# Performance work log

Measured on AMD Instinct MI355X. Metric: run time of the kernel, lower is better.

The kernel has to match this reference:

```python
import jax, jax.numpy as jnp
import numpy as np
import math

B, L, D, H = 2, 2048, 1024, 16
DH = D // H  # 64


def setup_inputs() -> dict:
    key = jax.random.key(0)
    ks = jax.random.split(key, 8)
    s = 1.0 / math.sqrt(D)
    return {
        "query": jax.random.normal(ks[0], (B, L, D), dtype=jnp.float32),
        "key": jax.random.normal(ks[1], (B, L, D), dtype=jnp.float32),
        "value": jax.random.normal(ks[2], (B, L, D), dtype=jnp.float32),
        "attn_mask": jax.random.bernoulli(ks[3], 0.1, (B, L, L)),  # True = masked
        "Wq": jax.random.normal(ks[4], (D, D), dtype=jnp.float32) * s,
        "Wk": jax.random.normal(ks[5], (D, D), dtype=jnp.float32) * s,
        "Wv": jax.random.normal(ks[6], (D, D), dtype=jnp.float32) * s,
        "Wo": jax.random.normal(ks[7], (D, D), dtype=jnp.float32) * s,
    }


def reference(query, key, value, attn_mask, Wq, Wk, Wv, Wo):
    # torch nn.Linear computes x @ W.T (bias=False here)
    def shape(x):
        b, l, _ = x.shape
        return x.reshape(b, l, H, DH).transpose(0, 2, 1, 3)  # [B,H,L,DH]

    q = shape(query @ Wq.T) / jnp.sqrt(jnp.float32(DH))
    k = shape(key @ Wk.T)
    v = shape(value @ Wv.T)

    scores = jnp.einsum("bhqd,bhkd->bhqk", q, k)  # [B,H,Q,K]
    if attn_mask is not None:
        scores = jnp.where(attn_mask[:, None, :, :], jnp.float32(-1e18), scores)
    attn = jax.nn.softmax(scores, axis=-1)
    # dropout p=0.0 (eval/deterministic) -> identity
    context = jnp.einsum("bhqk,bhkd->bhqd", attn, v)
    context = context.transpose(0, 2, 1, 3).reshape(query.shape[0], -1, D)
    output = context @ Wo.T
    top_attn = attn[:, 0, :, :]
    return output, top_attn
```

## Files before the change

kernel.cpp:

```cpp
#include <hip/hip_runtime.h>

#define BB 2
#define LL 2048
#define DD 1024
#define HH 16
#define DHH 64

typedef _Float16 f16;
typedef _Float16 f16x8 __attribute__((ext_vector_type(8)));
typedef _Float16 f16x4 __attribute__((ext_vector_type(4)));
typedef _Float16 f16x2 __attribute__((ext_vector_type(2)));
typedef float f32x4 __attribute__((ext_vector_type(4)));
typedef unsigned long long u64;

#define VWAIT(N) asm volatile("s_waitcnt vmcnt(" #N ")" ::: "memory")
#define SB0() __builtin_amdgcn_sched_barrier(0)

__device__ __forceinline__ void gload_lds16(const void* g, void* l) {
    __builtin_amdgcn_global_load_lds(
        (const __attribute__((address_space(1))) void*)g,
        (__attribute__((address_space(3))) void*)l, 16, 0, 0);
}

__device__ __forceinline__ f16x4 cvt4f(float4 v) {
    f16x4 o;
    o[0] = (f16)v.x; o[1] = (f16)v.y; o[2] = (f16)v.z; o[3] = (f16)v.w;
    return o;
}

__global__ void prep(const float* __restrict__ q, const float* __restrict__ k,
                     const float* __restrict__ v, const int* __restrict__ msk,
                     const float* __restrict__ wq, const float* __restrict__ wk,
                     const float* __restrict__ wv, const float* __restrict__ wo,
                     f16* __restrict__ bufQ, f16* __restrict__ bufK, f16* __restrict__ bufV,
                     f16* __restrict__ wh, u64* __restrict__ Mp, float scq) {
    const int tid = threadIdx.x;
    const int y = blockIdx.y;
    if (y == 0) {
        const int lane = tid & 63;
        int w = (blockIdx.x * 256 + tid) >> 6;
        const int nw = (1024 * 256) >> 6;
        for (; w < BB * LL * 32; w += nw) {
            int mv = msk[(size_t)w * 64 + lane];
            u64 bits = __ballot(mv != 0);
            if (lane == 0) {
                const int kt = w & 31;
                const int bq = w >> 5;
                const int qq = bq & 2047, b = bq >> 11;
                Mp[((size_t)b * 32 + kt) * LL + qq] = bits;
            }
        }
    } else if (y == 1) {
        int i = blockIdx.x * 256 + tid;
        const int stride = 1024 * 256;
        for (; i < 4 * 262144; i += stride) {
            const int sel = i >> 18, j = i & 262143;
            const float* s = sel == 0 ? wq : sel == 1 ? wk : sel == 2 ? wv : wo;
            ((f16x4*)wh)[i] = cvt4f(((const float4*)s)[j]);
        }
    } else {
        const float* s = y == 2 ? q : y == 3 ? k : v;
        f16* o = y == 2 ? bufQ : y == 3 ? bufK : bufV;
        const float sc = y == 2 ? scq : 1.0f;
        int i = blockIdx.x * 256 + tid;
        const int stride = 1024 * 256;
        for (; i < (int)(BB * LL * DD / 4); i += stride) {
            float4 vv = ((const float4*)s)[i];
            vv.x *= sc; vv.y *= sc; vv.z *= sc; vv.w *= sc;
            ((f16x4*)o)[i] = cvt4f(vv);
        }
    }
}

__global__ void cvt_kernel(const float* __restrict__ src, f16* __restrict__ dst, int n4, float sc) {
    int i = blockIdx.x * blockDim.x + threadIdx.x;
    const int stride = gridDim.x * blockDim.x;
    for (; i < n4; i += stride) {
        float4 v = ((const float4*)src)[i];
        v.x *= sc; v.y *= sc; v.z *= sc; v.w *= sc;
        ((f16x4*)dst)[i] = cvt4f(v);
    }
}
__global__ void cvt4_kernel(const float* __restrict__ a, const float* __restrict__ b,
                            const float* __restrict__ c, const float* __restrict__ d,
                            f16* __restrict__ dst, int n4) {
    const float* s = blockIdx.y == 0 ? a : blockIdx.y == 1 ? b : blockIdx.y == 2 ? c : d;
    f16* o = dst + (size_t)blockIdx.y * n4 * 4;
    int i = blockIdx.x * blockDim.x + threadIdx.x;
    const int stride = gridDim.x * blockDim.x;
    for (; i < n4; i += stride)
        ((f16x4*)o)[i] = cvt4f(((const float4*)s)[i]);
}
__global__ void pack_mask(const int* __restrict__ mask, u64* __restrict__ out, int nwords) {
    const int lane = threadIdx.x & 63;
    int w = (blockIdx.x * blockDim.x + threadIdx.x) >> 6;
    const int nw = (gridDim.x * blockDim.x) >> 6;
    for (; w < nwords; w += nw) {
        int mv = mask[(size_t)w * 64 + lane];
        u64 bits = __ballot(mv != 0);
        if (lane == 0) {
            const int kt = w & 31;
            const int bq = w >> 5;
            const int qq = bq & 2047, b = bq >> 11;
            out[((size_t)b * 32 + kt) * LL + qq] = bits;
        }
    }
}

__device__ __forceinline__ void gemm_core(const f16* __restrict__ A, const f16* __restrict__ W,
                                          f16* __restrict__ C, int z, int xb, int yb, char* lds) {
    const int tid = threadIdx.x, wid = tid >> 6, lane = tid & 63;
    const int m0 = yb * 128, n0 = xb * 128;
    const int lq = lane & 15, lg = lane >> 4;
    const int wm = (wid >> 1) << 6, wn = (wid & 1) << 6;
    f32x4 acc[4][4] = {};

    #pragma unroll
    for (int t = 0; t < 2; ++t)
        #pragma unroll
        for (int j = 0; j < 2; ++j) {
            const int ldsoff = (wid * 2 + j) << 10;
            const int o = ldsoff + lane * 16;
            const int row = o >> 6, c8 = (o >> 4) & 3;
            gload_lds16(A + (size_t)(m0 + row) * DD + t * 32 + c8 * 8, lds + t * 8192 + ldsoff);
            gload_lds16(W + (size_t)(n0 + row) * DD + t * 32 + c8 * 8, lds + 24576 + t * 8192 + ldsoff);
        }

    for (int kt = 0; kt < 32; ++kt) {
        VWAIT(4);
        SB0();
        __builtin_amdgcn_s_barrier();
        SB0();
        {
            const int nk = (kt + 2 < 32) ? kt + 2 : 31;
            const int nb = (kt + 2) % 3;
            #pragma unroll
            for (int j = 0; j < 2; ++j) {
                const int ldsoff = (wid * 2 + j) << 10;
                const int o = ldsoff + lane * 16;
                const int row = o >> 6, c8 = (o >> 4) & 3;
                gload_lds16(A + (size_t)(m0 + row) * DD + nk * 32 + c8 * 8,
                            lds + nb * 8192 + ldsoff);
                gload_lds16(W + (size_t)(n0 + row) * DD + nk * 32 + c8 * 8,
                            lds + 24576 + nb * 8192 + ldsoff);
            }
        }
        SB0();

        const int cb = kt % 3;
        const char* Ab = lds + cb * 8192;
        const char* Bb = lds + 24576 + cb * 8192;
        f16x8 af[4], bf[4];
        #pragma unroll
        for (int m = 0; m < 4; ++m)
            af[m] = *(const f16x8*)(Ab + (wm + m * 16 + lq) * 64 + lg * 16);
        #pragma unroll
        for (int n = 0; n < 4; ++n)
            bf[n] = *(const f16x8*)(Bb + (wn + n * 16 + lq) * 64 + lg * 16);
        __builtin_amdgcn_s_setprio(1);
        #pragma unroll
        for (int m = 0; m < 4; ++m)
            #pragma unroll
            for (int n = 0; n < 4; ++n)
                acc[m][n] = __builtin_amdgcn_mfma_f32_16x16x32_f16(af[m], bf[n], acc[m][n], 0, 0, 0);
        __builtin_amdgcn_s_setprio(0);
    }

    #pragma unroll
    for (int m = 0; m < 4; ++m)
        #pragma unroll
        for (int n = 0; n < 4; ++n)
            #pragma unroll
            for (int r = 0; r < 4; ++r) {
                const int row = m0 + wm + m * 16 + lg * 4 + r;
                const int col = n0 + wn + n * 16 + lq;
                const float val = acc[m][n][r];
                if (z < 2) {
                    C[(size_t)row * DD + col] = (f16)val;
                } else {
                    const int b = row >> 11, l = row & 2047;
                    const int h = col >> 6, dh = col & 63;
                    C[((size_t)((b * HH + h) * DHH + dh) << 11) + l] = (f16)val;
                }
            }
}

__global__ __launch_bounds__(256) void gemm_qkv(
        const f16* __restrict__ A0, const f16* __restrict__ A1, const f16* __restrict__ A2,
        const f16* __restrict__ W0, const f16* __restrict__ W1, const f16* __restrict__ W2,
        f16* __restrict__ C0, f16* __restrict__ C1, f16* __restrict__ C2) {
    __shared__ __align__(16) char lds[49152];
    const int bid = blockIdx.x;
    const int xcd = bid & 7, j = bid >> 3;
    const int p = xcd * 12 + (j >> 3);
    const int xb = j & 7;
    const int z = p >> 5, yb = p & 31;
    const f16* A = z == 0 ? A0 : z == 1 ? A1 : A2;
    const f16* W = z == 0 ? W0 : z == 1 ? W1 : W2;
    f16* C       = z == 0 ? C0 : z == 1 ? C1 : C2;
    gemm_core(A, W, C, z, xb, yb, lds);
}

__global__ __launch_bounds__(256) void gemm_one(const f16* __restrict__ A, const f16* __restrict__ W,
                                                f16* __restrict__ C, int z) {
    __shared__ __align__(16) char lds[49152];
    gemm_core(A, W, C, z, blockIdx.x, blockIdx.y, lds);
}

template<bool TOPF16>
__global__ __launch_bounds__(256) void finale(const f16* __restrict__ A, const f16* __restrict__ W,
                                              float* __restrict__ C, float* __restrict__ top,
                                              const void* __restrict__ src,
                                              const float* __restrict__ linvp) {
    __shared__ __align__(16) char lds[36864];
    const int tid = threadIdx.x;
    if (blockIdx.x >= 512) {
        int i = (blockIdx.x - 512) * 256 + tid;
        const int stride = 1024 * 256;
        if (TOPF16) {
            const f16x8* s8 = (const f16x8*)src;
            const int n = (int)((size_t)BB * LL * LL / 8);
            for (; i < n; i += stride) {
                f16x8 v = s8[i];
                const float linv = linvp[(i * 8) >> 11];
                float4 a, bq;
                a.x = (float)v[0] * linv; a.y = (float)v[1] * linv;
                a.z = (float)v[2] * linv; a.w = (float)v[3] * linv;
                bq.x = (float)v[4] * linv; bq.y = (float)v[5] * linv;
                bq.z = (float)v[6] * linv; bq.w = (float)v[7] * linv;
                ((float4*)top)[i * 2] = a;
                ((float4*)top)[i * 2 + 1] = bq;
            }
        } else {
            const int n = (int)((size_t)BB * LL * LL / 4);
            for (; i < n; i += stride) {
                float4 v = ((const float4*)top)[i];
                const float linv = linvp[(i * 4) >> 11];
                v.x = __builtin_amdgcn_exp2f(v.x) * linv;
                v.y = __builtin_amdgcn_exp2f(v.y) * linv;
                v.z = __builtin_amdgcn_exp2f(v.z) * linv;
                v.w = __builtin_amdgcn_exp2f(v.w) * linv;
                ((float4*)top)[i] = v;
            }
        }
        return;
    }
    const int bid = blockIdx.x;
    const int xcd = bid & 7, j = bid >> 3;
    const int yb = xcd * 4 + (j >> 4);
    const int xb = j & 15;
    const int wid = tid >> 6, lane = tid & 63;
    const int m0 = yb * 128, n0 = xb * 64;
    const int lq = lane & 15, lg = lane >> 4;
    const int wm = wid * 32;
    f32x4 acc[2][4] = {};

    #pragma unroll
    for (int t = 0; t < 2; ++t) {
        #pragma unroll
        for (int j2 = 0; j2 < 2; ++j2) {
            const int o = (j2 * 256 + tid) * 16;
            const int row = o >> 6, c8 = (o >> 4) & 3;
            gload_lds16(A + (size_t)(m0 + row) * DD + t * 32 + c8 * 8,
                        lds + t * 8192 + j2 * 4096 + (wid << 10));
        }
        {
            const int o = tid * 16;
            const int row = o >> 6, c8 = (o >> 4) & 3;
            gload_lds16(W + (size_t)(n0 + row) * DD + t * 32 + c8 * 8,
                        lds + 24576 + t * 4096 + (wid << 10));
        }
    }

    for (int kt = 0; kt < 32; ++kt) {
        VWAIT(3);
        SB0();
        __builtin_amdgcn_s_barrier();
        SB0();
        {
            const int nk = (kt + 2 < 32) ? kt + 2 : 31;
            const int nb = (kt + 2) % 3;
            #pragma unroll
            for (int j2 = 0; j2 < 2; ++j2) {
                const int o = (j2 * 256 + tid) * 16;
                const int row = o >> 6, c8 = (o >> 4) & 3;
                gload_lds16(A + (size_t)(m0 + row) * DD + nk * 32 + c8 * 8,
                            lds + nb * 8192 + j2 * 4096 + (wid << 10));
            }
            {
                const int o = tid * 16;
                const int row = o >> 6, c8 = (o >> 4) & 3;
                gload_lds16(W + (size_t)(n0 + row) * DD + nk * 32 + c8 * 8,
                            lds + 24576 + nb * 4096 + (wid << 10));
            }
        }
        SB0();

        const int cb = kt % 3;
        const char* Ab = lds + cb * 8192;
        const char* Bb = lds + 24576 + cb * 4096;
        f16x8 af[2], bf[4];
        #pragma unroll
        for (int m = 0; m < 2; ++m)
            af[m] = *(const f16x8*)(Ab + (wm + m * 16 + lq) * 64 + lg * 16);
        #pragma unroll
        for (int n = 0; n < 4; ++n)
            bf[n] = *(const f16x8*)(Bb + (n * 16 + lq) * 64 + lg * 16);
        __builtin_amdgcn_s_setprio(1);
        #pragma unroll
        for (int m = 0; m < 2; ++m)
            #pragma unroll
            for (int n = 0; n < 4; ++n)
                acc[m][n] = __builtin_amdgcn_mfma_f32_16x16x32_f16(af[m], bf[n], acc[m][n], 0, 0, 0);
        __builtin_amdgcn_s_setprio(0);
    }

    #pragma unroll
    for (int m = 0; m < 2; ++m)
        #pragma unroll
        for (int n = 0; n < 4; ++n)
            #pragma unroll
            for (int r = 0; r < 4; ++r) {
                const int row = m0 + wm + m * 16 + lg * 4 + r;
                const int col = n0 + n * 16 + lq;
                C[(size_t)row * DD + col] = acc[m][n][r];
            }
}

template<bool TOPF16>
__global__ __launch_bounds__(256) void attn_fwd(const f16* __restrict__ Qp, const f16* __restrict__ Kp,
                                                const f16* __restrict__ VTp,
                                                const u64* __restrict__ Mp,
                                                f16* __restrict__ Op, void* __restrict__ topout,
                                                float* __restrict__ statsLinv) {
    extern __shared__ char lds[];
    const int tid = threadIdx.x, wid = tid >> 6, lane = tid & 63;
    const int lq = lane & 15, lg = lane >> 4;
    const int bid = blockIdx.x;
    const int xcd = bid & 7, j = bid >> 3;
    const int bh = xcd * 4 + (j >> 5);
    const int qt = j & 31;
    const int b = bh >> 4, h = bh & 15;
    const bool topblk = (h == 0);
    const int qrow = qt * 64 + wid * 16 + lq;

    f16x8 qf[2];
    #pragma unroll
    for (int kk = 0; kk < 2; ++kk)
        qf[kk] = *(const f16x8*)(Qp + (size_t)(b * LL + qrow) * DD + h * 64 + (kk * 4 + lg) * 8);

    {
        #pragma unroll
        for (int jj = 0; jj < 2; ++jj) {
            const int o = (wid * 2 + jj) * 1024 + lane * 16;
            const int row = o >> 7, sc = ((o >> 4) & 7) ^ (row & 7);
            gload_lds16(Kp + (size_t)(b * LL + row) * DD + h * 64 + sc * 8,
                        lds + 8192 + (wid * 2 + jj) * 1024);
            gload_lds16(VTp + (size_t)((b * HH + h) * DHH + row) * LL + sc * 8,
                        lds + 24576 + (wid * 2 + jj) * 1024);
        }
    }

    float lsum = 0.f;
    f32x4 acc[4] = {};

    for (int kt = 0; kt < 32; ++kt) {
        if (topblk && kt > 0) { VWAIT(4); } else { VWAIT(0); }
        SB0();
        __builtin_amdgcn_s_barrier();
        SB0();
        const u64 cm = Mp[((size_t)b * 32 + kt) * LL + qrow];
        SB0();
        {
            const int nk = (kt + 1 < 32) ? kt + 1 : 31;
            const int nb = (kt + 1) & 1;
            #pragma unroll
            for (int jj = 0; jj < 2; ++jj) {
                const int o = (wid * 2 + jj) * 1024 + lane * 16;
                const int row = o >> 7, sc = ((o >> 4) & 7) ^ (row & 7);
                gload_lds16(Kp + (size_t)(b * LL + nk * 64 + row) * DD + h * 64 + sc * 8,
                            lds + 8192 + nb * 8192 + (wid * 2 + jj) * 1024);
                gload_lds16(VTp + (size_t)((b * HH + h) * DHH + row) * LL + nk * 64 + sc * 8,
                            lds + 24576 + nb * 8192 + (wid * 2 + jj) * 1024);
            }
        }
        SB0();

        const int cb = kt & 1;
        const char* Kb = lds + 8192 + cb * 8192;
        const char* Vb = lds + 24576 + cb * 8192;

        f32x4 s[4] = {};
        __builtin_amdgcn_s_setprio(1);
        #pragma unroll
        for (int f = 0; f < 4; ++f)
            #pragma unroll
            for (int kk = 0; kk < 2; ++kk) {
                const int co = (((kk * 4 + lg) ^ (lq & 7)) << 4);
                f16x8 kf = *(const f16x8*)(Kb + (f * 16 + lq) * 128 + co);
                s[f] = __builtin_amdgcn_mfma_f32_16x16x32_f16(kf, qf[kk], s[f], 0, 0, 0);
            }
        __builtin_amdgcn_s_setprio(0);

        const u64 wsh = cm >> (lg * 4);
        const unsigned lo = (unsigned)wsh, hi = (unsigned)(wsh >> 32);
        f16x4 ph[4];
        #pragma unroll
        for (int f = 0; f < 4; ++f) {
            const unsigned nib = ((f < 2) ? (lo >> (f * 16)) : (hi >> ((f - 2) * 16))) & 0xFu;
            #pragma unroll
            for (int r = 0; r < 4; ++r)
                if (nib & (1u << r)) s[f][r] = -1e18f;
            const float p0 = __builtin_amdgcn_exp2f(s[f][0]);
            const float p1 = __builtin_amdgcn_exp2f(s[f][1]);
            const float p2 = __builtin_amdgcn_exp2f(s[f][2]);
            const float p3 = __builtin_amdgcn_exp2f(s[f][3]);
            lsum += (p0 + p1) + (p2 + p3);
            f16x2 pa = __builtin_bit_cast(f16x2, __builtin_amdgcn_cvt_pkrtz(p0, p1));
            f16x2 pb = __builtin_bit_cast(f16x2, __builtin_amdgcn_cvt_pkrtz(p2, p3));
            ph[f][0] = pa[0]; ph[f][1] = pa[1]; ph[f][2] = pb[0]; ph[f][3] = pb[1];
        }

        if (topblk) {
            if (TOPF16) {
                f16* T = (f16*)topout;
                #pragma unroll
                for (int f = 0; f < 4; ++f)
                    *(f16x4*)(T + ((size_t)b * LL + qrow) * LL + kt * 64 + f * 16 + lg * 4) = ph[f];
            } else {
                float* T = (float*)topout;
                #pragma unroll
                for (int f = 0; f < 4; ++f)
                    *(f32x4*)(T + ((size_t)b * LL + qrow) * LL + kt * 64 + f * 16 + lg * 4) = s[f];
            }
        }

        #pragma unroll
        for (int f = 0; f < 4; ++f) {
            const int chunk = f * 2 + (lg >> 1);
            const int bo = ((chunk ^ (lq & 7)) << 4) + (lg & 1) * 8;
            *(f16x4*)(lds + (wid << 11) + lq * 128 + bo) = ph[f];
        }

        __builtin_amdgcn_s_setprio(1);
        #pragma unroll
        for (int kk = 0; kk < 2; ++kk) {
            const int co = (((kk * 4 + lg) ^ (lq & 7)) << 4);
            f16x8 pf = *(const f16x8*)(lds + (wid << 11) + lq * 128 + co);
            #pragma unroll
            for (int f = 0; f < 4; ++f) {
                f16x8 vf = *(const f16x8*)(Vb + (f * 16 + lq) * 128 + co);
                acc[f] = __builtin_amdgcn_mfma_f32_16x16x32_f16(vf, pf, acc[f], 0, 0, 0);
            }
        }
        __builtin_amdgcn_s_setprio(0);
    }

    lsum += __shfl_xor(lsum, 16);
    lsum += __shfl_xor(lsum, 32);
    const float linv = 1.f / lsum;
    #pragma unroll
    for (int f = 0; f < 4; ++f) {
        f16x4 ov;
        #pragma unroll
        for (int r = 0; r < 4; ++r) ov[r] = (f16)(acc[f][r] * linv);
        *(f16x4*)(Op + (size_t)(b * LL + qrow) * DD + h * 64 + f * 16 + lg * 4) = ov;
    }
    if (topblk && lg == 0) statsLinv[(size_t)b * LL + qrow] = linv;
}

extern "C" void kernel_launch(void* const* d_in, const int* in_sizes, int n_in,
                              void* d_out, int out_size, void* d_ws, size_t ws_size,
                              hipStream_t stream) {
    const float* q   = (const float*)d_in[0];
    const float* k   = (const float*)d_in[1];
    const float* v   = (const float*)d_in[2];
    const int*   msk = (const int*)d_in[3];
    const float* wq  = (const float*)d_in[4];
    const float* wk  = (const float*)d_in[5];
    const float* wv  = (const float*)d_in[6];
    const float* wo  = (const float*)d_in[7];
    float* out = (float*)d_out;

    const size_t NX = (size_t)BB * LL * DD;
    const size_t NW = (size_t)DD * DD;
    const int NMW = BB * LL * (LL / 64);
    const size_t NXo = NX;
    const float SCQ = 0.125f * 1.4426950408889634f;
    const int ALDS = 40960;

    f16* ws = (f16*)d_ws;
    const size_t needed = (6 * NX + 4 * NW) * 2 + (size_t)NMW * 8 + (size_t)BB * LL * 4;
    const bool fused = ws_size >= needed;

    if (fused) {
        f16* bufQ = ws;
        f16* bufK = bufQ + NX;
        f16* bufV = bufK + NX;
        f16* Op   = bufQ;
        f16* topP = bufK;
        f16* wh   = bufV + NX;
        f16* wqh = wh, *wkh = wh + NW, *wvh = wh + 2 * NW, *woh = wh + 3 * NW;
        f16* Qp  = wh + 4 * NW;
        f16* Kp  = Qp + NX;
        f16* VTp = Kp + NX;
        u64* Mp  = (u64*)(VTp + NX);
        float* statsLinv = (float*)(Mp + NMW);

        prep<<<dim3(1024, 5), 256, 0, stream>>>(q, k, v, msk, wq, wk, wv, wo,
                                                bufQ, bufK, bufV, wh, Mp, SCQ);
        gemm_qkv<<<768, 256, 0, stream>>>(bufQ, bufK, bufV, wqh, wkh, wvh, Qp, Kp, VTp);
        attn_fwd<true><<<1024, 256, ALDS, stream>>>(Qp, Kp, VTp, Mp, Op, topP, statsLinv);
        finale<true><<<1536, 256, 0, stream>>>(Op, woh, out, out + NXo, topP, statsLinv);
    } else {
        f16* bufA = ws;
        f16* wh   = bufA + NX;
        f16* wqh = wh, *wkh = wh + NW, *wvh = wh + 2 * NW, *woh = wh + 3 * NW;
        f16* Qp  = wh + 4 * NW;
        f16* Kp  = Qp + NX;
        f16* VTp = Kp + NX;
        u64* Mp  = (u64*)(VTp + NX);
        float* statsLinv = (float*)(Mp + NMW);

        pack_mask<<<256, 256, 0, stream>>>(msk, Mp, NMW);
        cvt4_kernel<<<dim3(128, 4), 256, 0, stream>>>(wq, wk, wv, wo, wh, (int)(NW / 4));
        cvt_kernel<<<2048, 256, 0, stream>>>(q, bufA, (int)(NX / 4), SCQ);
        gemm_one<<<dim3(8, 32), 256, 0, stream>>>(bufA, wqh, Qp, 0);
        cvt_kernel<<<2048, 256, 0, stream>>>(k, bufA, (int)(NX / 4), 1.f);
        gemm_one<<<dim3(8, 32), 256, 0, stream>>>(bufA, wkh, Kp, 1);
        cvt_kernel<<<2048, 256, 0, stream>>>(v, bufA, (int)(NX / 4), 1.f);
        gemm_one<<<dim3(8, 32), 256, 0, stream>>>(bufA, wvh, VTp, 2);
        attn_fwd<false><<<1024, 256, ALDS, stream>>>(Qp, Kp, VTp, Mp, bufA,
                                                     out + NXo, statsLinv);
        finale<false><<<1536, 256, 0, stream>>>(bufA, woh, out, out + NXo, out + NXo, statsLinv);
    }
}
```

Baseline: 161.2 us.

## Use 128-row query tiles with 8 waves and a 4-deep K/V pipeline

The attention kernel now runs 512 threads per block covering 128 query rows, so each K/V tile loaded into LDS serves twice as many queries. The loop handles two 64-key tiles per barrier with a 4-slot ring buffer, prefetching two tiles ahead. LDS per block doubles to 80 KB, set via hipFuncSetAttribute. This halves the block count to 512 and may lower occupancy.

```diff
diff --git a/kernel.cpp b/kernel.cpp
--- a/kernel.cpp
+++ b/kernel.cpp
@@ -328,7 +328,7 @@
 }
 
 template<bool TOPF16>
-__global__ __launch_bounds__(256) void attn_fwd(const f16* __restrict__ Qp, const f16* __restrict__ Kp,
+__global__ __launch_bounds__(512) void attn_fwd(const f16* __restrict__ Qp, const f16* __restrict__ Kp,
                                                 const f16* __restrict__ VTp,
                                                 const u64* __restrict__ Mp,
                                                 f16* __restrict__ Op, void* __restrict__ topout,
@@ -338,122 +338,123 @@
     const int lq = lane & 15, lg = lane >> 4;
     const int bid = blockIdx.x;
     const int xcd = bid & 7, j = bid >> 3;
-    const int bh = xcd * 4 + (j >> 5);
-    const int qt = j & 31;
+    const int bh = xcd * 4 + (j >> 4);
+    const int qt = j & 15;
     const int b = bh >> 4, h = bh & 15;
     const bool topblk = (h == 0);
-    const int qrow = qt * 64 + wid * 16 + lq;
+    const int qrow = qt * 128 + wid * 16 + lq;
+
+    const int srow = tid >> 3;
+    const int ssc = ((tid & 7) ^ (srow & 7));
+    const f16* ksrc = Kp + (size_t)(b * LL + srow) * DD + h * 64 + ssc * 8;
+    const f16* vsrc = VTp + (size_t)((b * HH + h) * DHH + srow) * LL + ssc * 8;
+    char* kdst = lds + 16384 + (wid << 10);
+    char* vdst = lds + 49152 + (wid << 10);
 
     f16x8 qf[2];
     #pragma unroll
     for (int kk = 0; kk < 2; ++kk)
         qf[kk] = *(const f16x8*)(Qp + (size_t)(b * LL + qrow) * DD + h * 64 + (kk * 4 + lg) * 8);
 
-    {
-        #pragma unroll
-        for (int jj = 0; jj < 2; ++jj) {
-            const int o = (wid * 2 + jj) * 1024 + lane * 16;
-            const int row = o >> 7, sc = ((o >> 4) & 7) ^ (row & 7);
-            gload_lds16(Kp + (size_t)(b * LL + row) * DD + h * 64 + sc * 8,
-                        lds + 8192 + (wid * 2 + jj) * 1024);
-            gload_lds16(VTp + (size_t)((b * HH + h) * DHH + row) * LL + sc * 8,
-                        lds + 24576 + (wid * 2 + jj) * 1024);
-        }
+    #pragma unroll
+    for (int t = 0; t < 2; ++t) {
+        gload_lds16(ksrc + (size_t)t * 64 * DD, kdst + t * 8192);
+        gload_lds16(vsrc + t * 64, vdst + t * 8192);
     }
 
     float lsum = 0.f;
     f32x4 acc[4] = {};
 
-    for (int kt = 0; kt < 32; ++kt) {
-        if (topblk && kt > 0) { VWAIT(4); } else { VWAIT(0); }
+    for (int it = 0; it < 16; ++it) {
+        const int kt0 = it * 2;
+        if (topblk && it > 0) { VWAIT(8); } else { VWAIT(0); }
         SB0();
         __builtin_amdgcn_s_barrier();
         SB0();
-        const u64 cm = Mp[((size_t)b * 32 + kt) * LL + qrow];
-        SB0();
-        {
-            const int nk = (kt + 1 < 32) ? kt + 1 : 31;
-            const int nb = (kt + 1) & 1;
-            #pragma unroll
-            for (int jj = 0; jj < 2; ++jj) {
-                const int o = (wid * 2 + jj) * 1024 + lane * 16;
-                const int row = o >> 7, sc = ((o >> 4) & 7) ^ (row & 7);
-                gload_lds16(Kp + (size_t)(b * LL + nk * 64 + row) * DD + h * 64 + sc * 8,
-                            lds + 8192 + nb * 8192 + (wid * 2 + jj) * 1024);
-                gload_lds16(VTp + (size_t)((b * HH + h) * DHH + row) * LL + nk * 64 + sc * 8,
-                            lds + 24576 + nb * 8192 + (wid * 2 + jj) * 1024);
-            }
-        }
-        SB0();
-
-        const int cb = kt & 1;
-        const char* Kb = lds + 8192 + cb * 8192;
-        const char* Vb = lds + 24576 + cb * 8192;
-
-        f32x4 s[4] = {};
-        __builtin_amdgcn_s_setprio(1);
-        #pragma unroll
-        for (int f = 0; f < 4; ++f)
+        const u64 cm0 = Mp[((size_t)b * 32 + kt0) * LL + qrow];
+        const u64 cm1 = Mp[((size_t)b * 32 + kt0 + 1) * LL + qrow];
+        SB0();
+        #pragma unroll
+        for (int t = 0; t < 2; ++t) {
+            const int nk = (kt0 + 2 + t < 32) ? kt0 + 2 + t : 31;
+            const int nb = (kt0 + 2 + t) & 3;
+            gload_lds16(ksrc + (size_t)nk * 64 * DD, kdst + nb * 8192);
+            gload_lds16(vsrc + nk * 64, vdst + nb * 8192);
+        }
+        SB0();
+
+        #pragma unroll
+        for (int t = 0; t < 2; ++t) {
+            const int cb = (kt0 + t) & 3;
+            const char* Kb = lds + 16384 + cb * 8192;
+            const char* Vb = lds + 49152 + cb * 8192;
+            const u64 cm = t == 0 ? cm0 : cm1;
+
+            f32x4 s[4] = {};
+            __builtin_amdgcn_s_setprio(1);
+            #pragma unroll
+            for (int f = 0; f < 4; ++f)
+                #pragma unroll
+                for (int kk = 0; kk < 2; ++kk) {
+                    const int co = (((kk * 4 + lg) ^ (lq & 7)) << 4);
+                    f16x8 kf = *(const f16x8*)(Kb + (f * 16 + lq) * 128 + co);
+                    s[f] = __builtin_amdgcn_mfma_f32_16x16x32_f16(kf, qf[kk], s[f], 0, 0, 0);
+                }
+            __builtin_amdgcn_s_setprio(0);
+
+            const u64 wsh = cm >> (lg * 4);
+            const unsigned lo = (unsigned)wsh, hi = (unsigned)(wsh >> 32);
+            f16x4 ph[4];
+            #pragma unroll
+            for (int f = 0; f < 4; ++f) {
+                const unsigned nib = ((f < 2) ? (lo >> (f * 16)) : (hi >> ((f - 2) * 16))) & 0xFu;
+                #pragma unroll
+                for (int r = 0; r < 4; ++r)
+                    if (nib & (1u << r)) s[f][r] = -1e18f;
+                const float p0 = __builtin_amdgcn_exp2f(s[f][0]);
+                const float p1 = __builtin_amdgcn_exp2f(s[f][1]);
+                const float p2 = __builtin_amdgcn_exp2f(s[f][2]);
+                const float p3 = __builtin_amdgcn_exp2f(s[f][3]);
+                lsum += (p0 + p1) + (p2 + p3);
+                f16x2 pa = __builtin_bit_cast(f16x2, __builtin_amdgcn_cvt_pkrtz(p0, p1));
+                f16x2 pb = __builtin_bit_cast(f16x2, __builtin_amdgcn_cvt_pkrtz(p2, p3));
+                ph[f][0] = pa[0]; ph[f][1] = pa[1]; ph[f][2] = pb[0]; ph[f][3] = pb[1];
+            }
+
+            if (topblk) {
+                if (TOPF16) {
+                    f16* T = (f16*)topout;
+                    #pragma unroll
+                    for (int f = 0; f < 4; ++f)
+                        *(f16x4*)(T + ((size_t)b * LL + qrow) * LL + (kt0 + t) * 64 + f * 16 + lg * 4) = ph[f];
+                } else {
+                    float* T = (float*)topout;
+                    #pragma unroll
+                    for (int f = 0; f < 4; ++f)
+                        *(f32x4*)(T + ((size_t)b * LL + qrow) * LL + (kt0 + t) * 64 + f * 16 + lg * 4) = s[f];
+                }
+            }
+
+            #pragma unroll
+            for (int f = 0; f < 4; ++f) {
+                const int chunk = f * 2 + (lg >> 1);
+                const int bo = ((chunk ^ (lq & 7)) << 4) + (lg & 1) * 8;
+                *(f16x4*)(lds + (wid << 11) + lq * 128 + bo) = ph[f];
+            }
+
+            __builtin_amdgcn_s_setprio(1);
             #pragma unroll
             for (int kk = 0; kk < 2; ++kk) {
                 const int co = (((kk * 4 + lg) ^ (lq & 7)) << 4);
-                f16x8 kf = *(const f16x8*)(Kb + (f * 16 + lq) * 128 + co);
-                s[f] = __builtin_amdgcn_mfma_f32_16x16x32_f16(kf, qf[kk], s[f], 0, 0, 0);
-            }
-        __builtin_amdgcn_s_setprio(0);
-
-        const u64 wsh = cm >> (lg * 4);
-        const unsigned lo = (unsigned)wsh, hi = (unsigned)(wsh >> 32);
-        f16x4 ph[4];
-        #pragma unroll
-        for (int f = 0; f < 4; ++f) {
-            const unsigned nib = ((f < 2) ? (lo >> (f * 16)) : (hi >> ((f - 2) * 16))) & 0xFu;
-            #pragma unroll
-            for (int r = 0; r < 4; ++r)
-                if (nib & (1u << r)) s[f][r] = -1e18f;
-            const float p0 = __builtin_amdgcn_exp2f(s[f][0]);
-            const float p1 = __builtin_amdgcn_exp2f(s[f][1]);
-            const float p2 = __builtin_amdgcn_exp2f(s[f][2]);
-            const float p3 = __builtin_amdgcn_exp2f(s[f][3]);
-            lsum += (p0 + p1) + (p2 + p3);
-            f16x2 pa = __builtin_bit_cast(f16x2, __builtin_amdgcn_cvt_pkrtz(p0, p1));
-            f16x2 pb = __builtin_bit_cast(f16x2, __builtin_amdgcn_cvt_pkrtz(p2, p3));
-            ph[f][0] = pa[0]; ph[f][1] = pa[1]; ph[f][2] = pb[0]; ph[f][3] = pb[1];
-        }
-
-        if (topblk) {
-            if (TOPF16) {
-                f16* T = (f16*)topout;
+                f16x8 pf = *(const f16x8*)(lds + (wid << 11) + lq * 128 + co);
                 #pragma unroll
-                for (int f = 0; f < 4; ++f)
-                    *(f16x4*)(T + ((size_t)b * LL + qrow) * LL + kt * 64 + f * 16 + lg * 4) = ph[f];
-            } else {
-                float* T = (float*)topout;
-                #pragma unroll
-                for (int f = 0; f < 4; ++f)
-                    *(f32x4*)(T + ((size_t)b * LL + qrow) * LL + kt * 64 + f * 16 + lg * 4) = s[f];
-            }
-        }
-
-        #pragma unroll
-        for (int f = 0; f < 4; ++f) {
-            const int chunk = f * 2 + (lg >> 1);
-            const int bo = ((chunk ^ (lq & 7)) << 4) + (lg & 1) * 8;
-            *(f16x4*)(lds + (wid << 11) + lq * 128 + bo) = ph[f];
-        }
-
-        __builtin_amdgcn_s_setprio(1);
-        #pragma unroll
-        for (int kk = 0; kk < 2; ++kk) {
-            const int co = (((kk * 4 + lg) ^ (lq & 7)) << 4);
-            f16x8 pf = *(const f16x8*)(lds + (wid << 11) + lq * 128 + co);
-            #pragma unroll
-            for (int f = 0; f < 4; ++f) {
-                f16x8 vf = *(const f16x8*)(Vb + (f * 16 + lq) * 128 + co);
-                acc[f] = __builtin_amdgcn_mfma_f32_16x16x32_f16(vf, pf, acc[f], 0, 0, 0);
-            }
-        }
-        __builtin_amdgcn_s_setprio(0);
+                for (int f = 0; f < 4; ++f) {
+                    f16x8 vf = *(const f16x8*)(Vb + (f * 16 + lq) * 128 + co);
+                    acc[f] = __builtin_amdgcn_mfma_f32_16x16x32_f16(vf, pf, acc[f], 0, 0, 0);
+                }
+            }
+            __builtin_amdgcn_s_setprio(0);
+        }
     }
 
     lsum += __shfl_xor(lsum, 16);
@@ -487,7 +488,12 @@
     const int NMW = BB * LL * (LL / 64);
     const size_t NXo = NX;
     const float SCQ = 0.125f * 1.4426950408889634f;
-    const int ALDS = 40960;
+    const int ALDS = 81920;
+
+    hipFuncSetAttribute(reinterpret_cast<const void*>(attn_fwd<true>),
+                        hipFuncAttributeMaxDynamicSharedMemorySize, ALDS);
+    hipFuncSetAttribute(reinterpret_cast<const void*>(attn_fwd<false>),
+                        hipFuncAttributeMaxDynamicSharedMemorySize, ALDS);
 
     f16* ws = (f16*)d_ws;
     const size_t needed = (6 * NX + 4 * NW) * 2 + (size_t)NMW * 8 + (size_t)BB * LL * 4;
@@ -510,7 +516,7 @@
         prep<<<dim3(1024, 5), 256, 0, stream>>>(q, k, v, msk, wq, wk, wv, wo,
                                                 bufQ, bufK, bufV, wh, Mp, SCQ);
         gemm_qkv<<<768, 256, 0, stream>>>(bufQ, bufK, bufV, wqh, wkh, wvh, Qp, Kp, VTp);
-        attn_fwd<true><<<1024, 256, ALDS, stream>>>(Qp, Kp, VTp, Mp, Op, topP, statsLinv);
+        attn_fwd<true><<<512, 512, ALDS, stream>>>(Qp, Kp, VTp, Mp, Op, topP, statsLinv);
         finale<true><<<1536, 256, 0, stream>>>(Op, woh, out, out + NXo, topP, statsLinv);
     } else {
         f16* bufA = ws;
@@ -530,8 +536,8 @@
         gemm_one<<<dim3(8, 32), 256, 0, stream>>>(bufA, wkh, Kp, 1);
         cvt_kernel<<<2048, 256, 0, stream>>>(v, bufA, (int)(NX / 4), 1.f);
         gemm_one<<<dim3(8, 32), 256, 0, stream>>>(bufA, wvh, VTp, 2);
-        attn_fwd<false><<<1024, 256, ALDS, stream>>>(Qp, Kp, VTp, Mp, bufA,
-                                                     out + NXo, statsLinv);
+        attn_fwd<false><<<512, 512, ALDS, stream>>>(Qp, Kp, VTp, Mp, bufA,
+                                                    out + NXo, statsLinv);
         finale<false><<<1536, 256, 0, stream>>>(bufA, woh, out, out + NXo, out + NXo, statsLinv);
     }
 }
```

After: 159.9 us. About the same (-0.8%).
